# Optimization experiments

Measured on AMD Instinct MI355X. Metric: run time of the kernel, lower is better.

The kernel has to match this reference:

```python
import jax, jax.numpy as jnp
import numpy as np

B, T, C, H = 4, 4096, 1024, 64


def setup_inputs() -> dict:
    key = jax.random.key(0)
    kx, kk, kq, kv = jax.random.split(key, 4)
    x = jax.random.normal(kx, (B, T, C), dtype=jnp.float32)
    # bias-free linear weights, stored as [in, out] so y = x @ W
    Wk = jax.random.normal(kk, (C, H), dtype=jnp.float32) * (C ** -0.5)
    Wq = jax.random.normal(kq, (C, H), dtype=jnp.float32) * (C ** -0.5)
    Wv = jax.random.normal(kv, (C, H), dtype=jnp.float32) * (C ** -0.5)
    return {"x": x, "Wk": Wk, "Wq": Wq, "Wv": Wv}


def reference(x, Wk, Wq, Wv):
    b, t, c = x.shape
    k = x @ Wk  # [B,T,H]
    q = x @ Wq
    v = x @ Wv
    # NOTE: original scales by C**-0.5 (num_embed), not head_size**-0.5
    wei = jnp.einsum('bqh,bkh->bqk', q, k) * (c ** -0.5)  # [B,T,T]
    causal = jnp.tril(jnp.ones((t, t), dtype=bool))
    wei = jnp.where(causal, wei, -jnp.inf)
    wei = jax.nn.softmax(wei, axis=-1)
    # dropout p=0.0 (eval) -> identity
    return jnp.einsum('bqk,bkh->bqh', wei, v)  # [B,T,H]
```

## Files before the change

kernel.cpp:

```cpp
#include <hip/hip_runtime.h>
#include <hip/hip_bf16.h>

typedef unsigned short u16;
typedef unsigned int u32;
using f32x4 = __attribute__((ext_vector_type(4))) float;
using s16x8 = __attribute__((ext_vector_type(8))) short;

#define BATCH 4
#define SEQ   4096
#define CDIM  1024
#define HDIM  64
#define QT_N  256

__device__ inline u16 f32_to_bf16(float f) {
    u32 u = __builtin_bit_cast(u32, f);
    u += 0x7FFFu + ((u >> 16) & 1u);
    return (u16)(u >> 16);
}
__device__ inline u32 pkbf16(float a, float b) {
    return (u32)f32_to_bf16(a) | ((u32)f32_to_bf16(b) << 16);
}
__device__ inline f32x4 mfma16(s16x8 a, s16x8 b, f32x4 c) {
    return __builtin_amdgcn_mfma_f32_16x16x32_bf16(a, b, c, 0, 0, 0);
}


__global__ __launch_bounds__(64) void wtrans_kernel(
        const float* __restrict__ Wk, const float* __restrict__ Wq,
        const float* __restrict__ Wv, u16* __restrict__ Wtf) {
    int bx = blockIdx.x;
    int nt = bx >> 5, kc = bx & 31;
    int lane = threadIdx.x;
    int l16 = lane & 15, qd = lane >> 4;
    int n = nt * 16 + l16;
    int a = n >> 6, h = n & 63;
    const float* src = (a == 0) ? Wk : (a == 1) ? Wq : Wv;
    float scale = (a == 1) ? 0.045084220027780106f : 1.0f;
    u32 p[4];
#pragma unroll
    for (int pp = 0; pp < 4; ++pp) {
        int k = kc * 32 + qd * 8 + pp * 2;
        p[pp] = pkbf16(src[k * HDIM + h] * scale, src[(k + 1) * HDIM + h] * scale);
    }
    uint4 u; u.x = p[0]; u.y = p[1]; u.z = p[2]; u.w = p[3];
    *(uint4*)&Wtf[(size_t)((nt * 32 + kc) * 64 + lane) * 8] = u;
}

__global__ __launch_bounds__(256, 2) void proj_kernel(
        const float* __restrict__ x, const u16* __restrict__ Wtf,
        u16* __restrict__ qf, u16* __restrict__ kf, u16* __restrict__ vf) {
    __shared__ __align__(16) u16 xs[32][1032];
    int t = threadIdx.x, lane = t & 63, w = t >> 6;
    int quad = lane >> 4, l16 = lane & 15;
    int row0 = blockIdx.x * 32;

    const float* xb = x + (size_t)row0 * CDIM;
#pragma unroll 4
    for (int i = 0; i < 32; ++i) {
        float4 f = *(const float4*)(xb + (size_t)i * CDIM + t * 4);
        uint2 u; u.x = pkbf16(f.x, f.y); u.y = pkbf16(f.z, f.w);
        *(uint2*)&xs[i][t * 4] = u;
    }
    __syncthreads();

    f32x4 acc[2][3];
#pragma unroll
    for (int m = 0; m < 2; ++m)
#pragma unroll
        for (int n = 0; n < 3; ++n) acc[m][n] = (f32x4){0.f, 0.f, 0.f, 0.f};

#pragma unroll 4
    for (int kc = 0; kc < 32; ++kc) {
        s16x8 a0 = *(const s16x8*)&xs[l16][kc * 32 + quad * 8];
        s16x8 a1 = *(const s16x8*)&xs[16 + l16][kc * 32 + quad * 8];
#pragma unroll
        for (int n = 0; n < 3; ++n) {
            int nt = w * 3 + n;
            s16x8 b = *(const s16x8*)&Wtf[(size_t)((nt * 32 + kc) * 64 + lane) * 8];
            acc[0][n] = mfma16(a0, b, acc[0][n]);
            acc[1][n] = mfma16(a1, b, acc[1][n]);
        }
    }
#pragma unroll
    for (int m = 0; m < 2; ++m) {
        int rbase = row0 + m * 16 + quad * 4;
        int bb = rbase >> 12, rl = rbase & 4095;
#pragma unroll
        for (int n = 0; n < 3; ++n) {
            int n0 = w * 48 + n * 16;
            if (n0 < 128) {
                u16* dst = (n0 < 64) ? kf : qf;
                int h = (n0 & 63) + l16;
                int tt16 = rl >> 4, hc = h >> 5, qd2 = (h >> 3) & 3, j = h & 7;
                size_t base = ((size_t)((bb * 256 + tt16) * 2 + hc) * 64
                               + qd2 * 16 + (rl & 15)) * 8 + j;
#pragma unroll
                for (int r = 0; r < 4; ++r)
                    dst[base + (size_t)r * 8] = f32_to_bf16(acc[m][n][r]);
            } else {
                int h0 = n0 - 128;
                int ht = h0 >> 4;
                int kc2 = rl >> 5, qdv = (rl >> 3) & 3, j0 = rl & 7;
                u32 lo = pkbf16(acc[m][n][0], acc[m][n][1]);
                u32 hi = pkbf16(acc[m][n][2], acc[m][n][3]);
                size_t base = ((size_t)((bb * 128 + kc2) * 4 + ht) * 64
                               + qdv * 16 + l16) * 8 + j0;
                uint2 u; u.x = lo; u.y = hi;
                *(uint2*)&vf[base] = u;
            }
        }
    }
}

__global__ __launch_bounds__(256, 4) void flash_kernel(
        const u16* __restrict__ qf, const u16* __restrict__ kf,
        const u16* __restrict__ vf, float* __restrict__ out) {
    __shared__ float cb[4][32][68];
    __shared__ float lb[4][32];
    int t = threadIdx.x, w = t >> 6, lane = t & 63;
    int quad = lane >> 4, l16 = lane & 15;
    int qt2 = (int)gridDim.x - 1 - (int)blockIdx.x;
    int b = blockIdx.y;

    const u16* qp0 = qf + ((size_t)((b * QT_N + qt2 * 2) * 2) * 64 + lane) * 8;
    const u16* qp1 = qp0 + 2 * 64 * 8;
    s16x8 bq[2][2];
    bq[0][0] = *(const s16x8*)qp0;
    bq[0][1] = *(const s16x8*)(qp0 + 512);
    bq[1][0] = *(const s16x8*)qp1;
    bq[1][1] = *(const s16x8*)(qp1 + 512);
    s16x8 ones;
#pragma unroll
    for (int j = 0; j < 8; ++j) ones[j] = (short)0x3F80;

    f32x4 o[2][4], o5[2];
#pragma unroll
    for (int tl = 0; tl < 2; ++tl) {
        o5[tl] = (f32x4){0.f, 0.f, 0.f, 0.f};
#pragma unroll
        for (int i = 0; i < 4; ++i) o[tl][i] = (f32x4){0.f, 0.f, 0.f, 0.f};
    }

    int nb = (qt2 * 32 + 32 + 63) >> 6;
    int iters = (nb + 3) >> 2;
    int rowq0 = qt2 * 32 + l16;
    const u16* kfb = kf + (size_t)b * 256 * 2 * 512;
    const u16* vfb = vf + (size_t)b * 128 * 4 * 512;
    int a0 = ((quad & 1) * 32 + l16) * 4;
    int a1 = a0 + 64;
    u32 msk = (quad < 2) ? 0xFFFFFFFFu : 0u;

    auto iteration = [&](int kb, bool domask) {
        f32x4 sT[2][4];
#pragma unroll
        for (int kt = 0; kt < 4; ++kt) {
            const u16* kp = kfb + ((size_t)((kb * 4 + kt) * 2) * 64 + lane) * 8;
            s16x8 k0 = *(const s16x8*)kp;
            s16x8 k1 = *(const s16x8*)(kp + 512);
            f32x4 z = (f32x4){0.f, 0.f, 0.f, 0.f};
            sT[0][kt] = mfma16(k1, bq[0][1], mfma16(k0, bq[0][0], z));
            sT[1][kt] = mfma16(k1, bq[1][1], mfma16(k0, bq[1][0], z));
        }
        u32 P01[2][4], P23[2][4];
#pragma unroll
        for (int tl = 0; tl < 2; ++tl) {
            int rowq = rowq0 + tl * 16;
#pragma unroll
            for (int kt = 0; kt < 4; ++kt) {
                float e[4];
#pragma unroll
                for (int r = 0; r < 4; ++r) {
                    float ev = __builtin_amdgcn_exp2f(sT[tl][kt][r]);
                    if (domask) {
                        int key = kb * 64 + kt * 16 + quad * 4 + r;
                        ev = (key > rowq) ? 0.f : ev;
                    }
                    e[r] = ev;
                }
                P01[tl][kt] = pkbf16(e[0], e[1]);
                P23[tl][kt] = pkbf16(e[2], e[3]);
            }
        }
#pragma unroll
        for (int c = 0; c < 2; ++c) {
            s16x8 vA[4];
#pragma unroll
            for (int ht = 0; ht < 4; ++ht)
                vA[ht] = *(const s16x8*)&vfb[((size_t)((kb * 2 + c) * 4 + ht) * 64
                                             + lane) * 8];
            int t0 = 2 * c, t1 = 2 * c + 1;
#pragma unroll
            for (int tl = 0; tl < 2; ++tl) {
                u32 x0 = (u32)__builtin_amdgcn_ds_bpermute(a0, (int)P01[tl][t0]);
                u32 y0 = (u32)__builtin_amdgcn_ds_bpermute(a0, (int)P01[tl][t1]);
                u32 x1 = (u32)__builtin_amdgcn_ds_bpermute(a0, (int)P23[tl][t0]);
                u32 y1 = (u32)__builtin_amdgcn_ds_bpermute(a0, (int)P23[tl][t1]);
                u32 x2 = (u32)__builtin_amdgcn_ds_bpermute(a1, (int)P01[tl][t0]);
                u32 y2 = (u32)__builtin_amdgcn_ds_bpermute(a1, (int)P01[tl][t1]);
                u32 x3 = (u32)__builtin_amdgcn_ds_bpermute(a1, (int)P23[tl][t0]);
                u32 y3 = (u32)__builtin_amdgcn_ds_bpermute(a1, (int)P23[tl][t1]);
                uint4 pu;
                pu.x = (x0 & msk) | (y0 & ~msk);
                pu.y = (x1 & msk) | (y1 & ~msk);
                pu.z = (x2 & msk) | (y2 & ~msk);
                pu.w = (x3 & msk) | (y3 & ~msk);
                s16x8 pb = __builtin_bit_cast(s16x8, pu);
#pragma unroll
                for (int ht = 0; ht < 4; ++ht)
                    o[tl][ht] = mfma16(vA[ht], pb, o[tl][ht]);
                o5[tl] = mfma16(ones, pb, o5[tl]);
            }
        }
    };

    for (int i = 0; i < iters - 1; ++i) iteration(4 * i + w, false);
    {
        int kb = 4 * (iters - 1) + w;
        if (kb < nb) iteration(kb, true);
    }
#pragma unroll
    for (int tl = 0; tl < 2; ++tl) {
#pragma unroll
        for (int ht = 0; ht < 4; ++ht)
#pragma unroll
            for (int r = 0; r < 4; ++r)
                cb[w][tl * 16 + l16][ht * 16 + quad * 4 + r] = o[tl][ht][r];
        if (quad == 0) lb[w][tl * 16 + l16] = o5[tl][0];
    }
    __syncthreads();
    int row = t >> 3, c0 = (t & 7) * 8;
    float l = lb[0][row] + lb[1][row] + lb[2][row] + lb[3][row];
    float rcp = 1.0f / l;
    float4 s0 = (float4){0.f, 0.f, 0.f, 0.f}, s1 = s0;
#pragma unroll
    for (int w4 = 0; w4 < 4; ++w4) {
        float4 p0 = *(const float4*)&cb[w4][row][c0];
        float4 p1 = *(const float4*)&cb[w4][row][c0 + 4];
        s0.x += p0.x; s0.y += p0.y; s0.z += p0.z; s0.w += p0.w;
        s1.x += p1.x; s1.y += p1.y; s1.z += p1.z; s1.w += p1.w;
    }
    s0.x *= rcp; s0.y *= rcp; s0.z *= rcp; s0.w *= rcp;
    s1.x *= rcp; s1.y *= rcp; s1.z *= rcp; s1.w *= rcp;
    float* op = &out[((size_t)(b * SEQ) + qt2 * 32 + row) * HDIM + c0];
    *(float4*)op = s0;
    *(float4*)(op + 4) = s1;
}

extern "C" void kernel_launch(void* const* d_in, const int* in_sizes, int n_in,
                              void* d_out, int out_size, void* d_ws, size_t ws_size,
                              hipStream_t stream) {
    const float* x  = (const float*)d_in[0];
    const float* Wk = (const float*)d_in[1];
    const float* Wq = (const float*)d_in[2];
    const float* Wv = (const float*)d_in[3];
    u16* wsu = (u16*)d_ws;
    u16* Wtf = wsu;
    u16* kf  = Wtf + 196608;
    u16* qf  = kf + 1048576;
    u16* vf  = qf + 1048576;
    float* out = (float*)d_out;

    hipLaunchKernelGGL(wtrans_kernel, dim3(384), dim3(64), 0, stream, Wk, Wq, Wv, Wtf);
    hipLaunchKernelGGL(proj_kernel, dim3(512), dim3(256), 0, stream, x, Wtf, qf, kf, vf);
    hipLaunchKernelGGL(flash_kernel, dim3(SEQ / 32, BATCH), dim3(256), 0, stream, qf, kf, vf, out);
}
```

Before: 147.2 us.

## Halve projection row tile and use eight waves per flash block

Result: faster. 133.5 us (-9.3%).

```diff
diff --git a/kernel.cpp b/kernel.cpp
--- a/kernel.cpp
+++ b/kernel.cpp
@@ -46,77 +46,70 @@
     *(uint4*)&Wtf[(size_t)((nt * 32 + kc) * 64 + lane) * 8] = u;
 }
 
-__global__ __launch_bounds__(256, 2) void proj_kernel(
+__global__ __launch_bounds__(256, 4) void proj_kernel(
         const float* __restrict__ x, const u16* __restrict__ Wtf,
         u16* __restrict__ qf, u16* __restrict__ kf, u16* __restrict__ vf) {
-    __shared__ __align__(16) u16 xs[32][1032];
+    __shared__ __align__(16) u16 xs[16][1032];
     int t = threadIdx.x, lane = t & 63, w = t >> 6;
     int quad = lane >> 4, l16 = lane & 15;
-    int row0 = blockIdx.x * 32;
+    int row0 = blockIdx.x * 16;
 
     const float* xb = x + (size_t)row0 * CDIM;
 #pragma unroll 4
-    for (int i = 0; i < 32; ++i) {
+    for (int i = 0; i < 16; ++i) {
         float4 f = *(const float4*)(xb + (size_t)i * CDIM + t * 4);
         uint2 u; u.x = pkbf16(f.x, f.y); u.y = pkbf16(f.z, f.w);
         *(uint2*)&xs[i][t * 4] = u;
     }
     __syncthreads();
 
-    f32x4 acc[2][3];
-#pragma unroll
-    for (int m = 0; m < 2; ++m)
-#pragma unroll
-        for (int n = 0; n < 3; ++n) acc[m][n] = (f32x4){0.f, 0.f, 0.f, 0.f};
+    f32x4 acc[3];
+#pragma unroll
+    for (int n = 0; n < 3; ++n) acc[n] = (f32x4){0.f, 0.f, 0.f, 0.f};
 
 #pragma unroll 4
     for (int kc = 0; kc < 32; ++kc) {
         s16x8 a0 = *(const s16x8*)&xs[l16][kc * 32 + quad * 8];
-        s16x8 a1 = *(const s16x8*)&xs[16 + l16][kc * 32 + quad * 8];
 #pragma unroll
         for (int n = 0; n < 3; ++n) {
             int nt = w * 3 + n;
             s16x8 b = *(const s16x8*)&Wtf[(size_t)((nt * 32 + kc) * 64 + lane) * 8];
-            acc[0][n] = mfma16(a0, b, acc[0][n]);
-            acc[1][n] = mfma16(a1, b, acc[1][n]);
-        }
-    }
-#pragma unroll
-    for (int m = 0; m < 2; ++m) {
-        int rbase = row0 + m * 16 + quad * 4;
-        int bb = rbase >> 12, rl = rbase & 4095;
-#pragma unroll
-        for (int n = 0; n < 3; ++n) {
-            int n0 = w * 48 + n * 16;
-            if (n0 < 128) {
-                u16* dst = (n0 < 64) ? kf : qf;
-                int h = (n0 & 63) + l16;
-                int tt16 = rl >> 4, hc = h >> 5, qd2 = (h >> 3) & 3, j = h & 7;
-                size_t base = ((size_t)((bb * 256 + tt16) * 2 + hc) * 64
-                               + qd2 * 16 + (rl & 15)) * 8 + j;
-#pragma unroll
-                for (int r = 0; r < 4; ++r)
-                    dst[base + (size_t)r * 8] = f32_to_bf16(acc[m][n][r]);
-            } else {
-                int h0 = n0 - 128;
-                int ht = h0 >> 4;
-                int kc2 = rl >> 5, qdv = (rl >> 3) & 3, j0 = rl & 7;
-                u32 lo = pkbf16(acc[m][n][0], acc[m][n][1]);
-                u32 hi = pkbf16(acc[m][n][2], acc[m][n][3]);
-                size_t base = ((size_t)((bb * 128 + kc2) * 4 + ht) * 64
-                               + qdv * 16 + l16) * 8 + j0;
-                uint2 u; u.x = lo; u.y = hi;
-                *(uint2*)&vf[base] = u;
-            }
-        }
-    }
-}
-
-__global__ __launch_bounds__(256, 4) void flash_kernel(
+            acc[n] = mfma16(a0, b, acc[n]);
+        }
+    }
+    int rbase = row0 + quad * 4;
+    int bb = rbase >> 12, rl = rbase & 4095;
+#pragma unroll
+    for (int n = 0; n < 3; ++n) {
+        int n0 = w * 48 + n * 16;
+        if (n0 < 128) {
+            u16* dst = (n0 < 64) ? kf : qf;
+            int h = (n0 & 63) + l16;
+            int tt16 = rl >> 4, hc = h >> 5, qd2 = (h >> 3) & 3, j = h & 7;
+            size_t base = ((size_t)((bb * 256 + tt16) * 2 + hc) * 64
+                           + qd2 * 16 + (rl & 15)) * 8 + j;
+#pragma unroll
+            for (int r = 0; r < 4; ++r)
+                dst[base + (size_t)r * 8] = f32_to_bf16(acc[n][r]);
+        } else {
+            int h0 = n0 - 128;
+            int ht = h0 >> 4;
+            int kc2 = rl >> 5, qdv = (rl >> 3) & 3, j0 = rl & 7;
+            u32 lo = pkbf16(acc[n][0], acc[n][1]);
+            u32 hi = pkbf16(acc[n][2], acc[n][3]);
+            size_t base = ((size_t)((bb * 128 + kc2) * 4 + ht) * 64
+                           + qdv * 16 + l16) * 8 + j0;
+            uint2 u; u.x = lo; u.y = hi;
+            *(uint2*)&vf[base] = u;
+        }
+    }
+}
+
+__global__ __launch_bounds__(512, 4) void flash_kernel(
         const u16* __restrict__ qf, const u16* __restrict__ kf,
         const u16* __restrict__ vf, float* __restrict__ out) {
-    __shared__ float cb[4][32][68];
-    __shared__ float lb[4][32];
+    __shared__ float cb[8][32][68];
+    __shared__ float lb[8][32];
     int t = threadIdx.x, w = t >> 6, lane = t & 63;
     int quad = lane >> 4, l16 = lane & 15;
     int qt2 = (int)gridDim.x - 1 - (int)blockIdx.x;
@@ -142,7 +135,7 @@
     }
 
     int nb = (qt2 * 32 + 32 + 63) >> 6;
-    int iters = (nb + 3) >> 2;
+    int iters = (nb + 7) >> 3;
     int rowq0 = qt2 * 32 + l16;
     const u16* kfb = kf + (size_t)b * 256 * 2 * 512;
     const u16* vfb = vf + (size_t)b * 128 * 4 * 512;
@@ -213,9 +206,9 @@
         }
     };
 
-    for (int i = 0; i < iters - 1; ++i) iteration(4 * i + w, false);
+    for (int i = 0; i < iters - 1; ++i) iteration(8 * i + w, false);
     {
-        int kb = 4 * (iters - 1) + w;
+        int kb = 8 * (iters - 1) + w;
         if (kb < nb) iteration(kb, true);
     }
 #pragma unroll
@@ -228,22 +221,18 @@
         if (quad == 0) lb[w][tl * 16 + l16] = o5[tl][0];
     }
     __syncthreads();
-    int row = t >> 3, c0 = (t & 7) * 8;
-    float l = lb[0][row] + lb[1][row] + lb[2][row] + lb[3][row];
+    int row = t >> 4, c0 = (t & 15) * 4;
+    float l = 0.f;
+    float4 s = (float4){0.f, 0.f, 0.f, 0.f};
+#pragma unroll
+    for (int w8 = 0; w8 < 8; ++w8) {
+        l += lb[w8][row];
+        float4 p = *(const float4*)&cb[w8][row][c0];
+        s.x += p.x; s.y += p.y; s.z += p.z; s.w += p.w;
+    }
     float rcp = 1.0f / l;
-    float4 s0 = (float4){0.f, 0.f, 0.f, 0.f}, s1 = s0;
-#pragma unroll
-    for (int w4 = 0; w4 < 4; ++w4) {
-        float4 p0 = *(const float4*)&cb[w4][row][c0];
-        float4 p1 = *(const float4*)&cb[w4][row][c0 + 4];
-        s0.x += p0.x; s0.y += p0.y; s0.z += p0.z; s0.w += p0.w;
-        s1.x += p1.x; s1.y += p1.y; s1.z += p1.z; s1.w += p1.w;
-    }
-    s0.x *= rcp; s0.y *= rcp; s0.z *= rcp; s0.w *= rcp;
-    s1.x *= rcp; s1.y *= rcp; s1.z *= rcp; s1.w *= rcp;
-    float* op = &out[((size_t)(b * SEQ) + qt2 * 32 + row) * HDIM + c0];
-    *(float4*)op = s0;
-    *(float4*)(op + 4) = s1;
+    s.x *= rcp; s.y *= rcp; s.z *= rcp; s.w *= rcp;
+    *(float4*)&out[((size_t)(b * SEQ) + qt2 * 32 + row) * HDIM + c0] = s;
 }
 
 extern "C" void kernel_launch(void* const* d_in, const int* in_sizes, int n_in,
@@ -261,6 +250,6 @@
     float* out = (float*)d_out;
 
     hipLaunchKernelGGL(wtrans_kernel, dim3(384), dim3(64), 0, stream, Wk, Wq, Wv, Wtf);
-    hipLaunchKernelGGL(proj_kernel, dim3(512), dim3(256), 0, stream, x, Wtf, qf, kf, vf);
-    hipLaunchKernelGGL(flash_kernel, dim3(SEQ / 32, BATCH), dim3(256), 0, stream, qf, kf, vf, out);
-}
+    hipLaunchKernelGGL(proj_kernel, dim3(1024), dim3(256), 0, stream, x, Wtf, qf, kf, vf);
+    hipLaunchKernelGGL(flash_kernel, dim3(SEQ / 32, BATCH), dim3(512), 0, stream, qf, kf, vf, out);
+}
```
